# Optimization experiments

Hardware: AMD Instinct MI355X
Metric: run time of the kernel (lower is better)

Reference implementation:

```python
import jax, jax.numpy as jnp
import numpy as np

N_NODES = 50000
N_EDGES = 1600000
N_GRAPHS = 64


def setup_inputs() -> dict:
    key = jax.random.key(0)
    ks = jax.random.split(key, 16)
    x = jax.random.normal(ks[0], (N_NODES, 900), dtype=jnp.float32)
    edge_index = jax.random.randint(ks[1], (2, N_EDGES), 0, N_NODES, dtype=jnp.int64)
    batch = jnp.sort(jax.random.randint(ks[2], (N_NODES,), 0, N_GRAPHS, dtype=jnp.int64))

    def lin(k, out_d, in_d):
        return jax.random.normal(k, (out_d, in_d), dtype=jnp.float32) / np.sqrt(in_d)

    return {
        "x": x, "edge_index": edge_index, "batch": batch,
        # SAGEConv1: lin_l (aggregated, with bias), lin_r (root, no bias)
        "W1l": lin(ks[3], 1024, 900), "b1": jnp.zeros((1024,), jnp.float32), "W1r": lin(ks[4], 1024, 900),
        # SAGEConv2
        "W2l": lin(ks[5], 2048, 1024), "b2": jnp.zeros((2048,), jnp.float32), "W2r": lin(ks[6], 2048, 1024),
        # MLP head
        "Wf1": lin(ks[7], 1024, 2048), "bf1": jnp.zeros((1024,), jnp.float32),
        "Wf2": lin(ks[8], 6, 1024), "bf2": jnp.zeros((6,), jnp.float32),
    }


def _sage_conv(x, src, dst, Wl, b, Wr):
    # mean aggregation of neighbor (source) features onto target nodes
    agg = jax.ops.segment_sum(x[src], dst, num_segments=N_NODES)
    deg = jax.ops.segment_sum(jnp.ones((src.shape[0],), x.dtype), dst, num_segments=N_NODES)
    mean = agg / jnp.maximum(deg, 1.0)[:, None]
    return mean @ Wl.T + b + x @ Wr.T


def reference(x, edge_index, batch, W1l, b1, W1r, W2l, b2, W2r, Wf1, bf1, Wf2, bf2):
    src, dst = edge_index[0], edge_index[1]
    h = jax.nn.relu(_sage_conv(x, src, dst, W1l, b1, W1r))   # [N, 1024]
    h = _sage_conv(h, src, dst, W2l, b2, W2r)                 # [N, 2048]
    pooled = jax.ops.segment_max(h, batch, num_segments=N_GRAPHS)  # [G, 2048]
    pooled = jnp.where(jnp.isfinite(pooled), pooled, 0.0)     # guard empty graphs
    out = jax.nn.relu(pooled @ Wf1.T + bf1) @ Wf2.T + bf2     # [G, 6]
    return out
```

## Files before the change

### kernel.cpp

```cpp
#include <hip/hip_runtime.h>

typedef unsigned short u16x8 __attribute__((ext_vector_type(8)));
typedef char i8x16 __attribute__((ext_vector_type(16)));
typedef int i32x4 __attribute__((ext_vector_type(4)));

constexpr int NN = 50000;
constexpr int NG = 64;
constexpr int MP = 50048;
constexpr int D0 = 900;
constexpr int K0 = 960;
constexpr int D1 = 1024;
constexpr int D2 = 2048;
constexpr int KC1 = 2 * K0;
constexpr int KC2 = 2 * D1;

__device__ __forceinline__ float bf2f(unsigned short u) {
  return __uint_as_float(((unsigned)u) << 16);
}
__device__ __forceinline__ unsigned short f2bf(float f) {
  unsigned x = __float_as_uint(f);
  return (unsigned short)((x + 0x7fffu + ((x >> 16) & 1u)) >> 16);
}

__device__ __forceinline__ void gl_lds16(const void* g, void* l) {
  __builtin_amdgcn_global_load_lds((const __attribute__((address_space(1))) void*)g,
                                   (__attribute__((address_space(3))) void*)l, 16, 0, 0);
}

__global__ __launch_bounds__(256) void cvt_x(const float* __restrict__ in,
                                             char* __restrict__ cat1,
                                             float* __restrict__ xscale) {
  int r = blockIdx.x;
  __shared__ float row[K0];
  __shared__ float smax[256];
  int t = threadIdx.x;
  float m = 0.f;
  for (int c = t; c < K0; c += 256) {
    float v = (r < NN && c < D0) ? in[(size_t)r * D0 + c] : 0.f;
    row[c] = v;
    m = fmaxf(m, fabsf(v));
  }
  smax[t] = m;
  __syncthreads();
  for (int dd = 128; dd; dd >>= 1) {
    if (t < dd) smax[t] = fmaxf(smax[t], smax[t + dd]);
    __syncthreads();
  }
  float mx = smax[0];
  float inv = mx > 0.f ? 127.f / mx : 0.f;
  char* dst = cat1 + (size_t)r * KC1 + K0;
  for (int c = t; c < K0; c += 256) dst[c] = (char)(int)rintf(row[c] * inv);
  if (t == 0) xscale[r] = mx * (1.f / 127.f);
}

__global__ __launch_bounds__(256) void wq_cat(const float* __restrict__ Wl,
                                              const float* __restrict__ Wr, int Cin, int KH,
                                              char* __restrict__ q, float* __restrict__ sc) {
  int r = blockIdx.x, t = threadIdx.x;
  __shared__ float smax[256];
  float m = 0.f;
  for (int c = t; c < Cin; c += 256) {
    m = fmaxf(m, fabsf(Wl[(size_t)r * Cin + c]));
    m = fmaxf(m, fabsf(Wr[(size_t)r * Cin + c]));
  }
  smax[t] = m;
  __syncthreads();
  for (int dd = 128; dd; dd >>= 1) {
    if (t < dd) smax[t] = fmaxf(smax[t], smax[t + dd]);
    __syncthreads();
  }
  float mx = smax[0];
  float inv = mx > 0.f ? 127.f / mx : 0.f;
  char* row = q + (size_t)r * 2 * KH;
  for (int c = t; c < KH; c += 256) {
    row[c]      = (c < Cin) ? (char)(int)rintf(Wl[(size_t)r * Cin + c] * inv) : 0;
    row[KH + c] = (c < Cin) ? (char)(int)rintf(Wr[(size_t)r * Cin + c] * inv) : 0;
  }
  if (t == 0) sc[r] = mx * (1.f / 127.f);
}

__global__ __launch_bounds__(256) void quant_rows(const unsigned short* __restrict__ in,
                                                  char* __restrict__ cat2,
                                                  float* __restrict__ scale) {
  int r = blockIdx.x;
  __shared__ float row[D1];
  __shared__ float smax[256];
  int t = threadIdx.x;
  float m = 0.f;
  for (int c = t; c < D1; c += 256) {
    float v = bf2f(in[(size_t)r * D1 + c]);
    row[c] = v;
    m = fmaxf(m, fabsf(v));
  }
  smax[t] = m;
  __syncthreads();
  for (int dd = 128; dd; dd >>= 1) {
    if (t < dd) smax[t] = fmaxf(smax[t], smax[t + dd]);
    __syncthreads();
  }
  float mx = smax[0];
  float inv = mx > 0.f ? 127.f / mx : 0.f;
  char* dst = cat2 + (size_t)r * KC2 + D1;
  for (int c = t; c < D1; c += 256) dst[c] = (char)(int)rintf(row[c] * inv);
  if (t == 0) scale[r] = mx * (1.f / 127.f);
}

__global__ void zero_i(int* p, int n) {
  int i = blockIdx.x * blockDim.x + threadIdx.x;
  if (i < n) p[i] = 0;
}
__global__ void count_k(const int* __restrict__ dst, int* __restrict__ deg, int E, int n) {
  int e = blockIdx.x * blockDim.x + threadIdx.x;
  if (e < E) {
    int d = dst[e];
    if ((unsigned)d < (unsigned)n) atomicAdd(&deg[d], 1);
  }
}
__global__ void scan1_k(const int* __restrict__ deg, int* __restrict__ off,
                        int* __restrict__ bsum, int n) {
  __shared__ int s[256];
  int t = threadIdx.x;
  int gid = blockIdx.x * 256 + t;
  int v = (gid < n) ? deg[gid] : 0;
  s[t] = v;
  __syncthreads();
  for (int d = 1; d < 256; d <<= 1) {
    int x = (t >= d) ? s[t - d] : 0;
    __syncthreads();
    s[t] += x;
    __syncthreads();
  }
  if (gid < n) off[gid] = s[t] - v;
  if (t == 255) bsum[blockIdx.x] = s[255];
}
__global__ void scan2_k(int* __restrict__ bsum, int nb) {
  __shared__ int s[256];
  int t = threadIdx.x;
  int v = (t < nb) ? bsum[t] : 0;
  s[t] = v;
  __syncthreads();
  for (int d = 1; d < 256; d <<= 1) {
    int x = (t >= d) ? s[t - d] : 0;
    __syncthreads();
    s[t] += x;
    __syncthreads();
  }
  if (t < nb) bsum[t] = s[t] - v;
  if (t == 255) bsum[nb] = s[255];
}
__global__ void scan3_k(int* __restrict__ off, const int* __restrict__ bsum, int n, int nb) {
  int gid = blockIdx.x * 256 + threadIdx.x;
  if (gid < n) off[gid] += bsum[gid >> 8];
  if (gid == 0) off[n] = bsum[nb];
}
__global__ void copy_i(const int* a, int* b, int n) {
  int i = blockIdx.x * blockDim.x + threadIdx.x;
  if (i < n) b[i] = a[i];
}
__global__ void fill_k(const int* __restrict__ src, const int* __restrict__ dst,
                       int* __restrict__ cursor, int* __restrict__ csr, int E, int n) {
  int e = blockIdx.x * blockDim.x + threadIdx.x;
  if (e < E) {
    int d = dst[e];
    if ((unsigned)d < (unsigned)n) {
      int p = atomicAdd(&cursor[d], 1);
      int s = src[e];
      if ((unsigned)s >= (unsigned)n) s = 0;
      csr[p] = s;
    }
  }
}

template <int K, int STRIDE>
__global__ __launch_bounds__(256) void agg_mean_i8w(char* __restrict__ cat,
                                                    const float* __restrict__ rscale,
                                                    const int* __restrict__ off,
                                                    const int* __restrict__ csr) {
  const int node = blockIdx.x * 4 + (threadIdx.x >> 6);
  const int lane = threadIdx.x & 63;
  const int d = lane * 16;
  const bool act = (d < K);
  const int e0 = off[node], e1 = off[node + 1];
  float a[16];
#pragma unroll
  for (int k = 0; k < 16; ++k) a[k] = 0.f;
  if (act) {
    const char* fp = cat + (size_t)K + d;
    int e = e0;
    for (; e + 7 < e1; e += 8) {
      int s0 = csr[e],     s1 = csr[e + 1], s2 = csr[e + 2], s3 = csr[e + 3];
      int s4 = csr[e + 4], s5 = csr[e + 5], s6 = csr[e + 6], s7 = csr[e + 7];
      i8x16 v0 = *(const i8x16*)(fp + (size_t)s0 * STRIDE);
      i8x16 v1 = *(const i8x16*)(fp + (size_t)s1 * STRIDE);
      i8x16 v2 = *(const i8x16*)(fp + (size_t)s2 * STRIDE);
      i8x16 v3 = *(const i8x16*)(fp + (size_t)s3 * STRIDE);
      i8x16 v4 = *(const i8x16*)(fp + (size_t)s4 * STRIDE);
      i8x16 v5 = *(const i8x16*)(fp + (size_t)s5 * STRIDE);
      i8x16 v6 = *(const i8x16*)(fp + (size_t)s6 * STRIDE);
      i8x16 v7 = *(const i8x16*)(fp + (size_t)s7 * STRIDE);
      float c0 = rscale[s0], c1 = rscale[s1], c2 = rscale[s2], c3 = rscale[s3];
      float c4 = rscale[s4], c5 = rscale[s5], c6 = rscale[s6], c7 = rscale[s7];
#pragma unroll
      for (int k = 0; k < 16; ++k) {
        a[k] += c0 * (float)v0[k] + c1 * (float)v1[k] + c2 * (float)v2[k] + c3 * (float)v3[k];
        a[k] += c4 * (float)v4[k] + c5 * (float)v5[k] + c6 * (float)v6[k] + c7 * (float)v7[k];
      }
    }
    for (; e < e1; ++e) {
      int s = csr[e];
      float c = rscale[s];
      i8x16 v = *(const i8x16*)(fp + (size_t)s * STRIDE);
#pragma unroll
      for (int k = 0; k < 16; ++k) a[k] += c * (float)v[k];
    }
  }
  if (act) {
    int deg = e1 - e0;
    float inv = 1.f / (float)(deg > 1 ? deg : 1);
    float sc = rscale[node];
    float qi = sc > 0.f ? 1.f / sc : 0.f;
    i8x16 q;
#pragma unroll
    for (int k = 0; k < 16; ++k) {
      float m = a[k] * inv * qi;
      m = fminf(fmaxf(rintf(m), -127.f), 127.f);
      q[k] = (char)(int)m;
    }
    *(i8x16*)&cat[(size_t)node * STRIDE + d] = q;
  }
}

template <int KP, int N, bool RELU>
__global__ __launch_bounds__(256, 5) void gemm_i8(const char* __restrict__ A,
                                                  const char* __restrict__ W,
                                                  const float* __restrict__ sA_,
                                                  const float* __restrict__ sW_,
                                                  const float* __restrict__ bias,
                                                  unsigned short* __restrict__ C) {
  __shared__ __align__(16) char smem[17408];
  char* sA = smem;
  char* sB = smem + 8192;
  float* sc0 = (float*)(smem + 16384);
  float* sc1 = sc0 + 128;

  const int gx = gridDim.x;
  const int nwg = gx * gridDim.y;
  const int flat = blockIdx.y * gx + blockIdx.x;
  int newid = flat;
  if ((nwg & 7) == 0) newid = (flat & 7) * (nwg >> 3) + (flat >> 3);
  const int bxi = newid % gx;
  const int byi = newid / gx;

  const int tid = threadIdx.x;
  const int wave = tid >> 6, lane = tid & 63;
  const int quad = lane >> 4, l16 = lane & 15;
  const int wm = (wave >> 1) * 64, wn = (wave & 1) * 64;
  const long long bm = (long long)byi * 128;
  const long long bn = (long long)bxi * 128;

  if (tid < 128) sc0[tid] = sA_[bm + tid];
  else sc1[tid - 128] = sW_[bn + tid - 128];

  const int srow = wave * 16 + (lane >> 2);
  const int skoff = (lane & 3) * 16;
  char* lA = &sA[wave * 1024 + lane * 16];
  char* lB = &sB[wave * 1024 + lane * 16];
  const char* gA = A + (bm + srow) * (long long)KP + skoff;
  const char* gW = W + (bn + srow) * (long long)KP + skoff;

  i32x4 iacc[4][4];
#pragma unroll
  for (int i = 0; i < 4; ++i)
#pragma unroll
    for (int j = 0; j < 4; ++j) iacc[i][j] = (i32x4){0, 0, 0, 0};

#pragma unroll 1
  for (int k0 = 0; k0 < KP; k0 += 64) {
    __syncthreads();
    gl_lds16(gA + k0, lA);
    gl_lds16(gA + k0 + (size_t)64 * KP, lA + 4096);
    gl_lds16(gW + k0, lB);
    gl_lds16(gW + k0 + (size_t)64 * KP, lB + 4096);
    __syncthreads();
    i32x4 af[4], bg[4];
#pragma unroll
    for (int i = 0; i < 4; ++i)
      af[i] = *(const i32x4*)&sA[(wm + 16 * i + l16) * 64 + quad * 16];
#pragma unroll
    for (int j = 0; j < 4; ++j)
      bg[j] = *(const i32x4*)&sB[(wn + 16 * j + l16) * 64 + quad * 16];
#pragma unroll
    for (int i = 0; i < 4; ++i)
#pragma unroll
      for (int j = 0; j < 4; ++j)
        iacc[i][j] = __builtin_amdgcn_mfma_i32_16x16x64_i8(af[i], bg[j], iacc[i][j], 0, 0, 0);
  }

  float rs[4][4], cs[4], bvj[4];
#pragma unroll
  for (int i = 0; i < 4; ++i)
#pragma unroll
    for (int r = 0; r < 4; ++r) rs[i][r] = sc0[wm + 16 * i + quad * 4 + r];
#pragma unroll
  for (int j = 0; j < 4; ++j) {
    const int coll = wn + 16 * j + l16;
    cs[j] = sc1[coll];
    bvj[j] = bias[bn + coll];
  }
  unsigned short* ct = (unsigned short*)smem;
  const int trow = tid >> 4;
  const int tcol = (tid & 15) * 8;
#pragma unroll
  for (int p = 0; p < 2; ++p) {
    __syncthreads();
    if ((wm >> 6) == p) {
#pragma unroll
      for (int i = 0; i < 4; ++i)
#pragma unroll
        for (int j = 0; j < 4; ++j)
#pragma unroll
          for (int r = 0; r < 4; ++r) {
            float v = (float)iacc[i][j][r] * rs[i][r] * cs[j] + bvj[j];
            if (RELU) v = fmaxf(v, 0.f);
            ct[(16 * i + quad * 4 + r) * 136 + wn + 16 * j + l16] = f2bf(v);
          }
    }
    __syncthreads();
#pragma unroll
    for (int s = 0; s < 4; ++s) {
      const int rl = s * 16 + trow;
      i32x4 vv = *(const i32x4*)&ct[rl * 136 + tcol];
      *(i32x4*)&C[(bm + p * 64 + rl) * (long long)N + bn + tcol] = vv;
    }
  }
}

__global__ void bounds_k(const int* __restrict__ batch, int* __restrict__ gstart, int n, int G) {
  int g = blockIdx.x * blockDim.x + threadIdx.x;
  if (g > G) return;
  int lo = 0, hi = n;
  while (lo < hi) {
    int mid = (lo + hi) >> 1;
    if (batch[mid] < g) lo = mid + 1; else hi = mid;
  }
  gstart[g] = lo;
}

__global__ void segmax_k(const unsigned short* __restrict__ h2b, const int* __restrict__ gstart,
                         float* __restrict__ pooled) {
  int g = blockIdx.x;
  int c = blockIdx.y * 256 + threadIdx.x;
  int i0 = gstart[g], i1 = gstart[g + 1];
  float m = -3.4e38f;
  for (int i = i0; i < i1; ++i) m = fmaxf(m, bf2f(h2b[(size_t)i * D2 + c]));
  if (i0 >= i1) m = 0.f;
  pooled[(size_t)g * D2 + c] = m;
}

__global__ void head1_k(const float* __restrict__ pooled, const float* __restrict__ Wf1,
                        const float* __restrict__ bf1, float* __restrict__ hid) {
  int g = blockIdx.x, chunk = blockIdx.y;
  __shared__ float sp[2048];
  for (int i = threadIdx.x; i < 2048; i += 256) sp[i] = pooled[(size_t)g * 2048 + i];
  __syncthreads();
  int wave = threadIdx.x >> 6, lane = threadIdx.x & 63;
  for (int oi = wave; oi < 64; oi += 4) {
    int o = chunk * 64 + oi;
    const float4* wr = (const float4*)&Wf1[(size_t)o * 2048];
    float s = 0.f;
    for (int c = lane; c < 512; c += 64) {
      float4 wv = wr[c];
      float4 pv = *(const float4*)&sp[c * 4];
      s += wv.x * pv.x + wv.y * pv.y + wv.z * pv.z + wv.w * pv.w;
    }
    for (int off = 32; off; off >>= 1) s += __shfl_down(s, off);
    if (lane == 0) hid[(size_t)g * 1024 + o] = fmaxf(s + bf1[o], 0.f);
  }
}
__global__ void head2_k(const float* __restrict__ hid, const float* __restrict__ Wf2,
                        const float* __restrict__ bf2, float* __restrict__ out) {
  int g = blockIdx.x, t = threadIdx.x;
  __shared__ float sh[1024];
  __shared__ float red[256];
  for (int i = t; i < 1024; i += 256) sh[i] = hid[(size_t)g * 1024 + i];
  __syncthreads();
  for (int o = 0; o < 6; ++o) {
    float s = 0.f;
    for (int k = t; k < 1024; k += 256) s += sh[k] * Wf2[o * 1024 + k];
    red[t] = s;
    __syncthreads();
    for (int d = 128; d; d >>= 1) {
      if (t < d) red[t] += red[t + d];
      __syncthreads();
    }
    if (t == 0) out[g * 6 + o] = red[0] + bf2[o];
    __syncthreads();
  }
}

extern "C" void kernel_launch(void* const* d_in, const int* in_sizes, int n_in,
                              void* d_out, int out_size, void* d_ws, size_t ws_size,
                              hipStream_t stream) {
  const float* x    = (const float*)d_in[0];
  const int* ei     = (const int*)d_in[1];
  const int* batch  = (const int*)d_in[2];
  const float* W1l  = (const float*)d_in[3];
  const float* b1   = (const float*)d_in[4];
  const float* W1r  = (const float*)d_in[5];
  const float* W2l  = (const float*)d_in[6];
  const float* b2   = (const float*)d_in[7];
  const float* W2r  = (const float*)d_in[8];
  const float* Wf1  = (const float*)d_in[9];
  const float* bf1  = (const float*)d_in[10];
  const float* Wf2  = (const float*)d_in[11];
  const float* bf2  = (const float*)d_in[12];
  float* out = (float*)d_out;

  const int E = in_sizes[1] / 2;
  const int* srcp = ei;
  const int* dstp = ei + E;
  const int NB = (MP + 255) / 256;

  char* w = (char*)d_ws;
  auto take = [&](size_t b) {
    void* p = (void*)w;
    w += (b + 255) & ~(size_t)255;
    return p;
  };
  char* cat1      = (char*)take((size_t)MP * KC1);
  char* cat2      = (char*)take((size_t)MP * KC2);
  unsigned short* h1b = (unsigned short*)take((size_t)MP * D1 * 2);
  unsigned short* h2b = (unsigned short*)take((size_t)MP * D2 * 2);
  char* wcat1     = (char*)take((size_t)D1 * KC1);
  char* wcat2     = (char*)take((size_t)D2 * KC2);
  float* xscale   = (float*)take((size_t)MP * 4);
  float* h1scale  = (float*)take((size_t)MP * 4);
  float* swc1     = (float*)take((size_t)D1 * 4);
  float* swc2     = (float*)take((size_t)D2 * 4);
  int* deg    = (int*)take((size_t)MP * 4);
  int* off    = (int*)take((size_t)(MP + 1) * 4);
  int* bsum   = (int*)take((size_t)(NB + 1) * 4);
  int* cursor = (int*)take((size_t)MP * 4);
  int* csr    = (int*)take((size_t)E * 4);
  int* gstart = (int*)take((size_t)(NG + 1) * 4);
  float* pooled = (float*)take((size_t)NG * D2 * 4);
  float* hid    = (float*)take((size_t)NG * 1024 * 4);

  cvt_x<<<MP, 256, 0, stream>>>(x, cat1, xscale);
  wq_cat<<<D1, 256, 0, stream>>>(W1l, W1r, D0, K0, wcat1, swc1);
  wq_cat<<<D2, 256, 0, stream>>>(W2l, W2r, D1, D1, wcat2, swc2);

  zero_i<<<(MP + 255) / 256, 256, 0, stream>>>(deg, MP);
  count_k<<<(E + 255) / 256, 256, 0, stream>>>(dstp, deg, E, NN);
  scan1_k<<<NB, 256, 0, stream>>>(deg, off, bsum, MP);
  scan2_k<<<1, 256, 0, stream>>>(bsum, NB);
  scan3_k<<<NB, 256, 0, stream>>>(off, bsum, MP, NB);
  copy_i<<<(MP + 255) / 256, 256, 0, stream>>>(off, cursor, MP);
  fill_k<<<(E + 255) / 256, 256, 0, stream>>>(srcp, dstp, cursor, csr, E, NN);

  agg_mean_i8w<K0, KC1><<<MP / 4, 256, 0, stream>>>(cat1, xscale, off, csr);
  gemm_i8<KC1, D1, true><<<dim3(D1 / 128, MP / 128), 256, 0, stream>>>(
      cat1, wcat1, xscale, swc1, b1, h1b);

  quant_rows<<<MP, 256, 0, stream>>>(h1b, cat2, h1scale);
  agg_mean_i8w<D1, KC2><<<MP / 4, 256, 0, stream>>>(cat2, h1scale, off, csr);
  gemm_i8<KC2, D2, false><<<dim3(D2 / 128, MP / 128), 256, 0, stream>>>(
      cat2, wcat2, h1scale, swc2, b2, h2b);

  bounds_k<<<1, 128, 0, stream>>>(batch, gstart, NN, NG);
  segmax_k<<<dim3(NG, D2 / 256), 256, 0, stream>>>(h2b, gstart, pooled);
  head1_k<<<dim3(NG, 16), 256, 0, stream>>>(pooled, Wf1, bf1, hid);
  head2_k<<<NG, 256, 0, stream>>>(hid, Wf2, bf2, out);
}
```

Measured before the change: 1.688 ms.

## Double-buffer int8 GEMM LDS tiles with XOR swizzle and prefetch overlap

The int8 MFMA GEMM now double-buffers its A/W tiles in LDS and prefetches the next K-slice with direct global-to-LDS loads while the current slice is computed. Explicit vmcnt/lgkmcnt waits and raw barriers replace the two __syncthreads per iteration. An XOR swizzle on the 16-byte column chunk is meant to cut LDS bank conflicts on fragment reads, and s_setprio raises priority around the MFMA block. LDS use doubles and the occupancy hint drops from 5 to 4 workgroups, which costs latency hiding.

```diff
diff --git a/kernel.cpp b/kernel.cpp
--- a/kernel.cpp
+++ b/kernel.cpp
@@ -231,16 +231,14 @@
 }
 
 template <int KP, int N, bool RELU>
-__global__ __launch_bounds__(256, 5) void gemm_i8(const char* __restrict__ A,
+__global__ __launch_bounds__(256, 4) void gemm_i8(const char* __restrict__ A,
                                                   const char* __restrict__ W,
                                                   const float* __restrict__ sA_,
                                                   const float* __restrict__ sW_,
                                                   const float* __restrict__ bias,
                                                   unsigned short* __restrict__ C) {
-  __shared__ __align__(16) char smem[17408];
-  char* sA = smem;
-  char* sB = smem + 8192;
-  float* sc0 = (float*)(smem + 16384);
+  __shared__ __align__(16) char smem[33792];
+  float* sc0 = (float*)(smem + 32768);
   float* sc1 = sc0 + 128;
 
   const int gx = gridDim.x;
@@ -262,11 +260,12 @@
   else sc1[tid - 128] = sW_[bn + tid - 128];
 
   const int srow = wave * 16 + (lane >> 2);
-  const int skoff = (lane & 3) * 16;
-  char* lA = &sA[wave * 1024 + lane * 16];
-  char* lB = &sB[wave * 1024 + lane * 16];
-  const char* gA = A + (bm + srow) * (long long)KP + skoff;
-  const char* gW = W + (bn + srow) * (long long)KP + skoff;
+  const int cswz = (lane & 3) ^ ((lane >> 3) & 3);
+  const int ldst = wave * 1024 + lane * 16;
+  const char* gA = A + (bm + srow) * (long long)KP + cswz * 16;
+  const char* gW = W + (bn + srow) * (long long)KP + cswz * 16;
+
+  const int rdoff = l16 * 64 + ((quad ^ ((l16 >> 1) & 3)) << 4);
 
   i32x4 iacc[4][4];
 #pragma unroll
@@ -274,28 +273,59 @@
 #pragma unroll
     for (int j = 0; j < 4; ++j) iacc[i][j] = (i32x4){0, 0, 0, 0};
 
+  constexpr int NT = KP / 64;
+
+  {
+    char* dA = smem + ldst;
+    gl_lds16(gA, dA);
+    gl_lds16(gA + (size_t)64 * KP, dA + 4096);
+    gl_lds16(gW, dA + 8192);
+    gl_lds16(gW + (size_t)64 * KP, dA + 12288);
+  }
+
 #pragma unroll 1
-  for (int k0 = 0; k0 < KP; k0 += 64) {
-    __syncthreads();
-    gl_lds16(gA + k0, lA);
-    gl_lds16(gA + k0 + (size_t)64 * KP, lA + 4096);
-    gl_lds16(gW + k0, lB);
-    gl_lds16(gW + k0 + (size_t)64 * KP, lB + 4096);
-    __syncthreads();
+  for (int t = 0; t < NT; ++t) {
+    const int cur = t & 1;
+    if (t + 1 < NT) {
+      char* dA = smem + (cur ^ 1) * 16384 + ldst;
+      const char* sa = gA + (size_t)(t + 1) * 64;
+      const char* sw = gW + (size_t)(t + 1) * 64;
+      gl_lds16(sa, dA);
+      gl_lds16(sa + (size_t)64 * KP, dA + 4096);
+      gl_lds16(sw, dA + 8192);
+      gl_lds16(sw + (size_t)64 * KP, dA + 12288);
+      asm volatile("s_waitcnt vmcnt(4)" ::: "memory");
+    } else {
+      asm volatile("s_waitcnt vmcnt(0)" ::: "memory");
+    }
+    __builtin_amdgcn_sched_barrier(0);
+    __builtin_amdgcn_s_barrier();
+    __builtin_amdgcn_sched_barrier(0);
+
+    const char* rb = smem + cur * 16384;
     i32x4 af[4], bg[4];
 #pragma unroll
     for (int i = 0; i < 4; ++i)
-      af[i] = *(const i32x4*)&sA[(wm + 16 * i + l16) * 64 + quad * 16];
+      af[i] = *(const i32x4*)&rb[(wm + 16 * i) * 64 + rdoff];
 #pragma unroll
     for (int j = 0; j < 4; ++j)
-      bg[j] = *(const i32x4*)&sB[(wn + 16 * j + l16) * 64 + quad * 16];
+      bg[j] = *(const i32x4*)&rb[8192 + (wn + 16 * j) * 64 + rdoff];
+
+    asm volatile("s_waitcnt lgkmcnt(0)" ::: "memory");
+    __builtin_amdgcn_sched_barrier(0);
+    __builtin_amdgcn_s_barrier();
+    __builtin_amdgcn_sched_barrier(0);
+
+    __builtin_amdgcn_s_setprio(1);
 #pragma unroll
     for (int i = 0; i < 4; ++i)
 #pragma unroll
       for (int j = 0; j < 4; ++j)
         iacc[i][j] = __builtin_amdgcn_mfma_i32_16x16x64_i8(af[i], bg[j], iacc[i][j], 0, 0, 0);
-  }
-
+    __builtin_amdgcn_s_setprio(0);
+  }
+
+  __syncthreads();
   float rs[4][4], cs[4], bvj[4];
 #pragma unroll
   for (int i = 0; i < 4; ++i)
```

New measurement: 1.666 ms. About the same (-1.3%).

## Double-buffer int8 GEMM mainloop with direct-to-register A loads and swizzled W tiles

Applied to the files above, without the earlier changes.

Restructures the int8 MFMA GEMM mainloop into a software-pipelined, double-buffered scheme. Only W tiles are staged in LDS, using an XOR swizzle to avoid bank conflicts, while A fragments are loaded straight from global into registers one K-step ahead. Explicit vmcnt waits, s_barrier and setprio are used to overlap loads with MFMAs, and MP is padded to a multiple of 256. The extra register buffers lower the occupancy hint from 5 to 3 waves, and the loop assumes an even number of K-tiles.

```diff
diff --git a/kernel.cpp b/kernel.cpp
--- a/kernel.cpp
+++ b/kernel.cpp
@@ -6,7 +6,7 @@
 
 constexpr int NN = 50000;
 constexpr int NG = 64;
-constexpr int MP = 50048;
+constexpr int MP = 50176;
 constexpr int D0 = 900;
 constexpr int K0 = 960;
 constexpr int D1 = 1024;
@@ -231,16 +231,14 @@
 }
 
 template <int KP, int N, bool RELU>
-__global__ __launch_bounds__(256, 5) void gemm_i8(const char* __restrict__ A,
+__global__ __launch_bounds__(256, 3) void gemm_i8(const char* __restrict__ A,
                                                   const char* __restrict__ W,
                                                   const float* __restrict__ sA_,
                                                   const float* __restrict__ sW_,
                                                   const float* __restrict__ bias,
                                                   unsigned short* __restrict__ C) {
-  __shared__ __align__(16) char smem[17408];
-  char* sA = smem;
-  char* sB = smem + 8192;
-  float* sc0 = (float*)(smem + 16384);
+  __shared__ __align__(16) char smem[18432];
+  float* sc0 = (float*)(smem + 17408);
   float* sc1 = sc0 + 128;
 
   const int gx = gridDim.x;
@@ -261,12 +259,13 @@
   if (tid < 128) sc0[tid] = sA_[bm + tid];
   else sc1[tid - 128] = sW_[bn + tid - 128];
 
-  const int srow = wave * 16 + (lane >> 2);
-  const int skoff = (lane & 3) * 16;
-  char* lA = &sA[wave * 1024 + lane * 16];
-  char* lB = &sB[wave * 1024 + lane * 16];
-  const char* gA = A + (bm + srow) * (long long)KP + skoff;
-  const char* gW = W + (bn + srow) * (long long)KP + skoff;
+  const int srow = tid >> 2;
+  const int cswz = (tid & 3) ^ ((tid >> 3) & 3);
+  const char* gW0 = W + (bn + srow) * (long long)KP + cswz * 16;
+
+  const char* aptr = A + (bm + wm + l16) * (long long)KP + (quad << 4);
+
+  const int rdoff = (quad ^ ((l16 >> 1) & 3)) << 4;
 
   i32x4 iacc[4][4];
 #pragma unroll
@@ -274,27 +273,56 @@
 #pragma unroll
     for (int j = 0; j < 4; ++j) iacc[i][j] = (i32x4){0, 0, 0, 0};
 
+  constexpr int NT = KP / 64;
+  i32x4 afP[4], afQ[4], bg[4];
+
+  {
+    char* d = smem + (tid << 4);
+    gl_lds16(gW0, d);
+    gl_lds16(gW0 + (size_t)64 * KP, d + 4096);
+#pragma unroll
+    for (int i = 0; i < 4; ++i)
+      afP[i] = *(const i32x4*)(aptr + (size_t)(16 * i) * KP);
+  }
+
+#define KSTEP(T, AFU, AFL, CUR)                                                   \
+  {                                                                               \
+    if ((T) + 1 < NT) {                                                           \
+      char* d = smem + ((CUR) ^ 1) * 8192 + (tid << 4);                           \
+      const char* sw = gW0 + (size_t)((T) + 1) * 64;                              \
+      gl_lds16(sw, d);                                                            \
+      gl_lds16(sw + (size_t)64 * KP, d + 4096);                                   \
+      const char* sa = aptr + (size_t)((T) + 1) * 64;                             \
+      _Pragma("unroll") for (int i = 0; i < 4; ++i)                               \
+          AFL[i] = *(const i32x4*)(sa + (size_t)(16 * i) * KP);                   \
+      asm volatile("s_waitcnt vmcnt(6)" ::: "memory");                            \
+    } else {                                                                      \
+      asm volatile("s_waitcnt vmcnt(0)" ::: "memory");                            \
+    }                                                                             \
+    __builtin_amdgcn_sched_barrier(0);                                            \
+    __builtin_amdgcn_s_barrier();                                                 \
+    __builtin_amdgcn_sched_barrier(0);                                            \
+    const char* rb = smem + (CUR) * 8192;                                         \
+    _Pragma("unroll") for (int j = 0; j < 4; ++j)                                 \
+        bg[j] = *(const i32x4*)&rb[(wn + 16 * j + l16) * 64 + rdoff];             \
+    __builtin_amdgcn_s_setprio(1);                                                \
+    _Pragma("unroll") for (int i = 0; i < 4; ++i)                                 \
+      _Pragma("unroll") for (int j = 0; j < 4; ++j)                               \
+          iacc[i][j] = __builtin_amdgcn_mfma_i32_16x16x64_i8(AFU[i], bg[j],       \
+                                                             iacc[i][j], 0, 0, 0);\
+    __builtin_amdgcn_s_setprio(0);                                                \
+    __builtin_amdgcn_sched_barrier(0);                                            \
+    asm volatile("s_waitcnt lgkmcnt(0)" ::: "memory");                            \
+    __builtin_amdgcn_s_barrier();                                                 \
+    __builtin_amdgcn_sched_barrier(0);                                            \
+  }
+
 #pragma unroll 1
-  for (int k0 = 0; k0 < KP; k0 += 64) {
-    __syncthreads();
-    gl_lds16(gA + k0, lA);
-    gl_lds16(gA + k0 + (size_t)64 * KP, lA + 4096);
-    gl_lds16(gW + k0, lB);
-    gl_lds16(gW + k0 + (size_t)64 * KP, lB + 4096);
-    __syncthreads();
-    i32x4 af[4], bg[4];
-#pragma unroll
-    for (int i = 0; i < 4; ++i)
-      af[i] = *(const i32x4*)&sA[(wm + 16 * i + l16) * 64 + quad * 16];
-#pragma unroll
-    for (int j = 0; j < 4; ++j)
-      bg[j] = *(const i32x4*)&sB[(wn + 16 * j + l16) * 64 + quad * 16];
-#pragma unroll
-    for (int i = 0; i < 4; ++i)
-#pragma unroll
-      for (int j = 0; j < 4; ++j)
-        iacc[i][j] = __builtin_amdgcn_mfma_i32_16x16x64_i8(af[i], bg[j], iacc[i][j], 0, 0, 0);
-  }
+  for (int t = 0; t < NT; t += 2) {
+    KSTEP(t, afP, afQ, 0);
+    KSTEP(t + 1, afQ, afP, 1);
+  }
+#undef KSTEP
 
   float rs[4][4], cs[4], bvj[4];
 #pragma unroll
```

New measurement: 1.956 ms. +15.9%, slower.
